# Optimization experiments

Measured on AMD Instinct MI355X. Metric: run time of the kernel, lower is better.

## Reference

```python
import jax, jax.numpy as jnp
import numpy as np

N_CVS = 4096
FEAT = 128
BATCH = 8192
K = 15
EPSILON = 0.9
E_MIN = 0.9 ** 10


def setup_inputs() -> dict:
    key = jax.random.key(0)
    k1, k2, k3 = jax.random.split(key, 3)
    x = jax.random.normal(k1, (BATCH, FEAT), dtype=jnp.float32)
    labels = jax.random.randint(k2, (BATCH,), 0, N_CVS, dtype=jnp.int64 if jax.config.jax_enable_x64 else jnp.int32)
    cvs = jax.random.normal(k3, (N_CVS, FEAT), dtype=jnp.float32)
    # module state buffers: identity-initialized edge / connectedness matrices
    edges = jnp.eye(N_CVS, dtype=jnp.float32)
    cv_connectedness = jnp.eye(N_CVS, dtype=jnp.float32)
    return {"x": x, "cvs": cvs, "edges": edges, "cv_connectedness": cv_connectedness, "labels": labels}


def reference(x, cvs, edges, cv_connectedness, labels):
    B = x.shape[0]
    N = cvs.shape[0]
    # squared pairwise distances (same ordering as cdist; x_cvs = cdist**2)
    d2 = (jnp.sum(x * x, axis=1)[:, None]
          + jnp.sum(cvs * cvs, axis=1)[None, :]
          - 2.0 * (x @ cvs.T))
    d2 = jnp.maximum(d2, 0.0)  # [B, N]

    # k nearest codevectors per sample (smallest distance first)
    _, knn = jax.lax.top_k(-d2, K)        # [B, K]
    closest = knn[:, 0]                    # [B]

    # visits per codevector (Counter over closest)
    visits = jnp.zeros((N,), dtype=jnp.float32).at[closest].add(1.0)
    # encounters[i, j] = visits[i]
    encounters = jnp.broadcast_to(visits[:, None], (N, N))

    # closest_cv_encounters[closest[i], knn[i, k]] += 1
    rows = jnp.repeat(closest, K)
    cols = knn.reshape(-1)
    cce = jnp.zeros((N, N), dtype=jnp.float32).at[rows, cols].add(1.0)

    existence = cce > 0
    enc = jnp.maximum(encounters - cce, 0.0)

    # edge update (state): refresh visited edges, exponentially decay others
    edges_new = jnp.maximum(edges, existence.astype(edges.dtype))
    edges_new = edges_new * (EPSILON ** enc)
    edges_new = jnp.where(edges_new < E_MIN, 0.0, edges_new)

    # margin loss
    d_pos = jnp.sum((x - cvs[labels]) ** 2, axis=1)                  # [B]
    neigh_mask = (edges_new > 0) & (cv_connectedness < 1)            # [N, N]
    d_neg = d2 * neigh_mask[labels].astype(d2.dtype)                 # [B, N]
    e_neg = jnp.exp(-0.001 * d_neg) * (d_neg > 0)
    w = e_neg / jnp.sum(e_neg, axis=1, keepdims=True)
    w = jnp.where(jnp.isnan(w), 0.0, w)
    w = jax.lax.stop_gradient(w)
    mu = d_pos - jnp.sum(w * d_neg, axis=1)
    loss = jnp.sum(jnp.maximum(mu, 0.0)) / B
    return loss
```

## Files before the change

kernel.cpp:

```cpp
#include <hip/hip_runtime.h>
#include <math.h>

#define N_CVS   4096
#define FEAT    128
#define BATCH   8192
#define KNN_K   15
#define E_MIN_F 0.34867844f

typedef __attribute__((ext_vector_type(8))) short bf16x8;
typedef __attribute__((ext_vector_type(4))) float f32x4;
typedef __attribute__((ext_vector_type(4))) unsigned int u32x4;

__global__ void cvtnorm_kernel(const float* __restrict__ x, const float* __restrict__ cvs,
                               unsigned short* __restrict__ xb, unsigned short* __restrict__ cb,
                               float* __restrict__ x2, float* __restrict__ c2) {
    size_t tid = (size_t)blockIdx.x * 256 + threadIdx.x;
    size_t f = tid * 8;
    const float* src; unsigned short* dst; float* ndst; size_t row;
    if (f < (size_t)BATCH * FEAT) { src = x + f; dst = xb + f; row = f >> 7; ndst = x2 + row; }
    else {
        size_t g = f - (size_t)BATCH * FEAT;
        src = cvs + g; dst = cb + g; row = g >> 7; ndst = c2 + row;
    }
    float4 v0 = ((const float4*)src)[0];
    float4 v1 = ((const float4*)src)[1];
    float vv[8] = {v0.x, v0.y, v0.z, v0.w, v1.x, v1.y, v1.z, v1.w};
    bf16x8 o;
    float s = 0.f;
    #pragma unroll
    for (int i = 0; i < 8; ++i) {
        unsigned u = __float_as_uint(vv[i]);
        o[i] = (short)((u + 0x7fffu + ((u >> 16) & 1u)) >> 16);
        s += vv[i] * vv[i];
    }
    *(bf16x8*)dst = o;
    #pragma unroll
    for (int off = 1; off < 16; off <<= 1) s += __shfl_xor(s, off, 64);
    if ((threadIdx.x & 15) == 0) *ndst = s;
}

#define LROW 272
#define TROW 132
__global__ __launch_bounds__(256) void mfma_d2_kernel(
        const unsigned short* __restrict__ xb, const unsigned short* __restrict__ cb,
        const float* __restrict__ x2g, const float* __restrict__ c2g,
        float* __restrict__ d2) {
    __shared__ __align__(16) char lds[2 * 128 * LROW];
    char* Al = lds;
    char* Bl = lds + 128 * LROW;
    const int bi = blockIdx.y * 128;
    const int bj = blockIdx.x * 128;
    const int t  = threadIdx.x;

    #pragma unroll
    for (int i = 0; i < 8; ++i) {
        int f = t + i * 256;
        int row = f >> 4, g = f & 15;
        ulonglong2 va = *(const ulonglong2*)((const char*)(xb + (size_t)(bi + row) * FEAT) + g * 16);
        *(ulonglong2*)(Al + row * LROW + g * 16) = va;
        ulonglong2 vb = *(const ulonglong2*)((const char*)(cb + (size_t)(bj + row) * FEAT) + g * 16);
        *(ulonglong2*)(Bl + row * LROW + g * 16) = vb;
    }
    __syncthreads();

    const int lane = t & 63;
    const int wave = t >> 6;
    const int wr = (wave >> 1) * 64;
    const int wc = (wave & 1) * 64;
    const int l15 = lane & 15, quad = lane >> 4;

    f32x4 acc[4][4];
    #pragma unroll
    for (int i = 0; i < 4; ++i)
        #pragma unroll
        for (int j = 0; j < 4; ++j)
            acc[i][j] = (f32x4){0.f, 0.f, 0.f, 0.f};

    #pragma unroll
    for (int ks = 0; ks < 4; ++ks) {
        bf16x8 a[4], b[4];
        #pragma unroll
        for (int s = 0; s < 4; ++s) {
            a[s] = *(const bf16x8*)(Al + (wr + s * 16 + l15) * LROW + ks * 64 + quad * 16);
            b[s] = *(const bf16x8*)(Bl + (wc + s * 16 + l15) * LROW + ks * 64 + quad * 16);
        }
        #pragma unroll
        for (int si = 0; si < 4; ++si)
            #pragma unroll
            for (int sj = 0; sj < 4; ++sj)
                acc[si][sj] = __builtin_amdgcn_mfma_f32_16x16x32_bf16(a[si], b[sj], acc[si][sj], 0, 0, 0);
    }

    float c2v[4];
    #pragma unroll
    for (int sj = 0; sj < 4; ++sj) c2v[sj] = c2g[bj + wc + sj * 16 + l15];
    __syncthreads();
    float* tile = (float*)lds;
    #pragma unroll
    for (int si = 0; si < 4; ++si) {
        #pragma unroll
        for (int r = 0; r < 4; ++r) {
            int mloc = wr + si * 16 + quad * 4 + r;
            float xv = x2g[bi + mloc];
            #pragma unroll
            for (int sj = 0; sj < 4; ++sj) {
                float v = fmaxf(xv + c2v[sj] - 2.0f * acc[si][sj][r], 0.0f);
                tile[mloc * TROW + wc + sj * 16 + l15] = v;
            }
        }
    }
    __syncthreads();
    #pragma unroll
    for (int i = 0; i < 16; ++i) {
        int s4  = t + i * 256;
        int row = s4 >> 5;
        int c4  = (s4 & 31) * 4;
        float4 v = *(const float4*)&tile[row * TROW + c4];
        *(float4*)(d2 + (size_t)(bi + row) * N_CVS + bj + c4) = v;
    }
}

__global__ __launch_bounds__(256, 3) void topk_kernel(const float* __restrict__ d2,
                                                      int* __restrict__ visits,
                                                      unsigned int* __restrict__ cce8) {
    __shared__ unsigned long long cand[4][64];
    const int wv   = threadIdx.x >> 6;
    const int wid  = blockIdx.x * 4 + wv;
    const int lane = threadIdx.x & 63;
    const float* row = d2 + (size_t)wid * N_CVS;

    float4 v[16];
    #pragma unroll
    for (int i = 0; i < 16; ++i)
        v[i] = *(const float4*)(row + lane * 4 + i * 256);

    float mn = fminf(fminf(v[0].x, v[0].y), fminf(v[0].z, v[0].w));
    #pragma unroll
    for (int i = 1; i < 16; ++i)
        mn = fminf(mn, fminf(fminf(v[i].x, v[i].y), fminf(v[i].z, v[i].w)));

    float s = mn;
    #pragma unroll
    for (int k = 2; k <= 64; k <<= 1) {
        #pragma unroll
        for (int j = k >> 1; j > 0; j >>= 1) {
            float o = __shfl_xor(s, j, 64);
            bool lower = ((lane & j) == 0);
            bool asc   = ((lane & k) == 0);
            float lo = fminf(s, o), hi = fmaxf(s, o);
            s = (lower == asc) ? lo : hi;
        }
    }
    float T = __shfl(s, 15, 64);

    unsigned long long* cbuf = cand[wv];
    int base = 0;
    #pragma unroll
    for (int i = 0; i < 16; ++i) {
        float vv[4] = {v[i].x, v[i].y, v[i].z, v[i].w};
        #pragma unroll
        for (int c = 0; c < 4; ++c) {
            bool p = (vv[c] <= T);
            unsigned long long mask = __ballot(p);
            if (p) {
                int pos = base + __popcll(mask & ((1ULL << lane) - 1ULL));
                if (pos < 64)
                    cbuf[pos] = ((unsigned long long)__float_as_uint(vv[c]) << 32)
                              | (unsigned)(lane * 4 + i * 256 + c);
            }
            base += __popcll(mask);
        }
    }
    __builtin_amdgcn_wave_barrier();

    int knnv[KNN_K];
    if (base <= 64) {
        unsigned long long key = (lane < base) ? cbuf[lane] : ~0ULL;
        #pragma unroll
        for (int r = 0; r < KNN_K; ++r) {
            unsigned long long m = key;
            #pragma unroll
            for (int off = 32; off > 0; off >>= 1) {
                unsigned long long o = __shfl_xor(m, off, 64);
                m = (o < m) ? o : m;
            }
            knnv[r] = (int)(unsigned)(m & 0xffffffffu);
            if (key == m) key = ~0ULL;
        }
    } else {
        unsigned long long heap[15];
        #pragma unroll
        for (int k = 0; k < 15; ++k) heap[k] = ~0ULL;
        for (int i = 0; i < 16; ++i) {
            int j0 = lane * 4 + i * 256;
            float4 f4 = *(const float4*)(row + j0);
            float vv[4] = {f4.x, f4.y, f4.z, f4.w};
            #pragma unroll
            for (int c = 0; c < 4; ++c) {
                unsigned long long key =
                    ((unsigned long long)__float_as_uint(vv[c]) << 32) | (unsigned)(j0 + c);
                if (key < heap[14]) {
                    heap[14] = key;
                    #pragma unroll
                    for (int k = 14; k > 0; --k) {
                        unsigned long long a = heap[k-1], b = heap[k];
                        bool sw = b < a;
                        heap[k-1] = sw ? b : a;
                        heap[k]   = sw ? a : b;
                    }
                }
            }
        }
        #pragma unroll
        for (int r = 0; r < KNN_K; ++r) {
            unsigned long long cd = heap[0];
            unsigned long long m = cd;
            #pragma unroll
            for (int off = 32; off > 0; off >>= 1) {
                unsigned long long o = __shfl_xor(m, off, 64);
                m = (o < m) ? o : m;
            }
            knnv[r] = (int)(unsigned)(m & 0xffffffffu);
            if (cd == m) {
                #pragma unroll
                for (int k = 0; k < 14; ++k) heap[k] = heap[k+1];
                heap[14] = ~0ULL;
            }
        }
    }

    if (lane == 0) {
        int closest = knnv[0];
        atomicAdd(&visits[closest], 1);
        size_t cbase = (size_t)closest * N_CVS;
        #pragma unroll
        for (int k = 0; k < KNN_K; ++k) {
            size_t idx = cbase + knnv[k];
            atomicAdd((int*)&cce8[idx >> 2], 1 << ((idx & 3) * 8));
        }
    }
}

__global__ __launch_bounds__(256) void bits_kernel(
        const unsigned int* __restrict__ cce8, const int* __restrict__ visits,
        const float* __restrict__ edges, const float* __restrict__ conn,
        unsigned short* __restrict__ bits16) {
    const int row = blockIdx.x;
    const int t   = threadIdx.x;
    const int vis = visits[row];
    size_t eb = (size_t)row * N_CVS + t * 16;
    f32x4 e[4];
    #pragma unroll
    for (int q = 0; q < 4; ++q) e[q] = ((const f32x4*)(edges + eb))[q];
    u32x4 cw = ((const u32x4*)(cce8 + (size_t)row * 1024))[t];

    unsigned pre = 0;
    #pragma unroll
    for (int q = 0; q < 4; ++q) {
        #pragma unroll
        for (int s = 0; s < 4; ++s) {
            int cc = (cw[q] >> (s * 8)) & 0xff;
            float ev = e[q][s];
            float ex = (cc > 0) ? fmaxf(ev, 1.0f) : ev;
            bool p;
            if (ex == 1.0f) {
                p = (vis - cc) <= 9;
            } else if (ex > 0.0f) {
                float enc = fmaxf((float)(vis - cc), 0.0f);
                p = ex * powf(0.9f, enc) >= E_MIN_F;
            } else {
                p = false;
            }
            pre |= (unsigned)p << (q * 4 + s);
        }
    }
    unsigned m = 0;
    #pragma unroll
    for (int q = 0; q < 4; ++q) {
        unsigned pn = (pre >> (q * 4)) & 0xfu;
        if (pn) {
            f32x4 cv = ((const f32x4*)(conn + eb))[q];
            #pragma unroll
            for (int s = 0; s < 4; ++s)
                if (((pn >> s) & 1u) && (cv[s] < 1.0f)) m |= 1u << (q * 4 + s);
        }
    }
    bits16[(size_t)row * 256 + t] = (unsigned short)m;
}

__global__ void loss_kernel(const float* __restrict__ d2,
                            const unsigned long long* __restrict__ bits,
                            const int* __restrict__ labels, float* __restrict__ partial) {
    int wid  = blockIdx.x * 4 + (threadIdx.x >> 6);
    int lane = threadIdx.x & 63;
    int l = labels[wid];
    const unsigned long long* rb = bits + (size_t)l * 64;
    const float* row = d2 + (size_t)wid * N_CVS;
    float se = 0.f, sed = 0.f;
    unsigned long long w = rb[lane];
    while (w) {
        int c = __builtin_ctzll(w);
        w &= w - 1;
        int j = lane * 64 + c;
        float d = row[j];
        if (d > 0.f) {
            float ee = __expf(-0.001f * d);
            se += ee; sed += ee * d;
        }
    }
    #pragma unroll
    for (int off = 32; off > 0; off >>= 1) {
        se  += __shfl_xor(se,  off, 64);
        sed += __shfl_xor(sed, off, 64);
    }
    if (lane == 0) {
        float dpos = row[l];
        float wsum = se > 0.f ? sed / se : 0.f;
        float mu = dpos - wsum;
        partial[wid] = (mu > 0.f) ? mu : 0.f;
    }
}

__global__ void reduce_kernel(const float* __restrict__ partial, float* __restrict__ out) {
    int t = threadIdx.x;
    float s = 0.f;
    #pragma unroll
    for (int i = 0; i < BATCH / 256; ++i) s += partial[t + i * 256];
    #pragma unroll
    for (int off = 32; off > 0; off >>= 1) s += __shfl_xor(s, off, 64);
    __shared__ float wsum[4];
    if ((t & 63) == 0) wsum[t >> 6] = s;
    __syncthreads();
    if (t == 0) out[0] = (wsum[0] + wsum[1] + wsum[2] + wsum[3]) * (1.0f / BATCH);
}

extern "C" void kernel_launch(void* const* d_in, const int* in_sizes, int n_in,
                              void* d_out, int out_size, void* d_ws, size_t ws_size,
                              hipStream_t stream) {
    const float* x      = (const float*)d_in[0];
    const float* cvs    = (const float*)d_in[1];
    const float* edges  = (const float*)d_in[2];
    const float* conn   = (const float*)d_in[3];
    const int*   labels = (const int*)d_in[4];

    char* p = (char*)d_ws;
    float* d2 = (float*)p;                  p += (size_t)BATCH * N_CVS * 4;
    int* visits = (int*)p;                  p += (size_t)N_CVS * 4;
    unsigned int* cce8 = (unsigned int*)p;  p += (size_t)N_CVS * N_CVS;
    unsigned long long* bits = (unsigned long long*)p;
                                            p += (size_t)N_CVS * 64 * 8;
    float* x2 = (float*)p;                  p += (size_t)BATCH * 4;
    float* c2 = (float*)p;                  p += (size_t)N_CVS * 4;
    unsigned short* xb = (unsigned short*)p; p += (size_t)BATCH * FEAT * 2;
    unsigned short* cb = (unsigned short*)p; p += (size_t)N_CVS * FEAT * 2;
    float* partial = (float*)p;             p += (size_t)BATCH * 4;

    hipMemsetAsync(visits, 0, (size_t)N_CVS * 4 + (size_t)N_CVS * N_CVS, stream);

    cvtnorm_kernel<<<(BATCH + N_CVS) * FEAT / 8 / 256, 256, 0, stream>>>(x, cvs, xb, cb, x2, c2);
    mfma_d2_kernel<<<dim3(N_CVS / 128, BATCH / 128), 256, 0, stream>>>(xb, cb, x2, c2, d2);
    topk_kernel   <<<BATCH / 4, 256, 0, stream>>>(d2, visits, cce8);
    bits_kernel   <<<N_CVS, 256, 0, stream>>>(
                      cce8, visits, edges, conn, (unsigned short*)bits);
    loss_kernel   <<<BATCH / 4, 256, 0, stream>>>(d2, bits, labels, partial);
    reduce_kernel <<<1, 256, 0, stream>>>(partial, (float*)d_out);
}
```

Baseline: 219.0 us.

## Fuse distance GEMM with streaming top-k and recompute loss distances on the fly

The bf16 MFMA distance computation is merged with k-nearest selection. Each 512-thread block keeps 32 x rows resident, streams codevector tiles through a double-buffered LDS, and keeps a running top-15 list per row using a shared candidate buffer with a threshold. This removes the 128 MB d2 matrix write and re-read. The loss kernel now recomputes the needed distances in fp32 directly from x and cvs for neighbour-mask bits only, so it no longer depends on d2. The cost is a per-tile __syncthreads loop with a serial insertion by 32 threads, low MFMA work per tile, and only 256 blocks.

```diff
diff --git a/kernel.cpp b/kernel.cpp
--- a/kernel.cpp
+++ b/kernel.cpp
@@ -10,6 +10,7 @@
 typedef __attribute__((ext_vector_type(8))) short bf16x8;
 typedef __attribute__((ext_vector_type(4))) float f32x4;
 typedef __attribute__((ext_vector_type(4))) unsigned int u32x4;
+typedef unsigned long long ull;
 
 __global__ void cvtnorm_kernel(const float* __restrict__ x, const float* __restrict__ cvs,
                                unsigned short* __restrict__ xb, unsigned short* __restrict__ cb,
@@ -39,203 +40,138 @@
     if ((threadIdx.x & 15) == 0) *ndst = s;
 }
 
-#define LROW 272
-#define TROW 132
-__global__ __launch_bounds__(256) void mfma_d2_kernel(
+#define LROW  272
+#define BROWS 32
+#define CAP   64
+#define NTILE (N_CVS / 128)
+
+__global__ __launch_bounds__(512, 2) void mfma_topk_kernel(
         const unsigned short* __restrict__ xb, const unsigned short* __restrict__ cb,
         const float* __restrict__ x2g, const float* __restrict__ c2g,
-        float* __restrict__ d2) {
-    __shared__ __align__(16) char lds[2 * 128 * LROW];
-    char* Al = lds;
-    char* Bl = lds + 128 * LROW;
-    const int bi = blockIdx.y * 128;
-    const int bj = blockIdx.x * 128;
+        int* __restrict__ visits, unsigned int* __restrict__ cce8) {
+    __shared__ __align__(16) char Bl[2][128 * LROW];
+    __shared__ __align__(16) char Al[BROWS * LROW];
+    __shared__ ull cand[BROWS][CAP];
+    __shared__ ull kT[BROWS];
+    __shared__ int cnt[BROWS];
+    __shared__ int ofl[BROWS];
+
     const int t  = threadIdx.x;
-
-    #pragma unroll
-    for (int i = 0; i < 8; ++i) {
-        int f = t + i * 256;
-        int row = f >> 4, g = f & 15;
-        ulonglong2 va = *(const ulonglong2*)((const char*)(xb + (size_t)(bi + row) * FEAT) + g * 16);
-        *(ulonglong2*)(Al + row * LROW + g * 16) = va;
-        ulonglong2 vb = *(const ulonglong2*)((const char*)(cb + (size_t)(bj + row) * FEAT) + g * 16);
-        *(ulonglong2*)(Bl + row * LROW + g * 16) = vb;
-    }
+    const int bi = blockIdx.x * BROWS;
+
+    {
+        int row = t >> 4, g = t & 15;
+        *(ulonglong2*)(Al + row * LROW + g * 16) =
+            *(const ulonglong2*)((const char*)(xb + (size_t)(bi + row) * FEAT) + g * 16);
+    }
+    #pragma unroll
+    for (int i = 0; i < 4; ++i) {
+        int f = t + i * 512, row = f >> 4, g = f & 15;
+        *(ulonglong2*)(Bl[0] + row * LROW + g * 16) =
+            *(const ulonglong2*)((const char*)(cb + (size_t)row * FEAT) + g * 16);
+    }
+    if (t < BROWS) { cnt[t] = 0; kT[t] = ~0ULL; ofl[t] = 0; }
     __syncthreads();
 
     const int lane = t & 63;
-    const int wave = t >> 6;
-    const int wr = (wave >> 1) * 64;
-    const int wc = (wave & 1) * 64;
-    const int l15 = lane & 15, quad = lane >> 4;
-
-    f32x4 acc[4][4];
-    #pragma unroll
-    for (int i = 0; i < 4; ++i)
-        #pragma unroll
-        for (int j = 0; j < 4; ++j)
-            acc[i][j] = (f32x4){0.f, 0.f, 0.f, 0.f};
-
-    #pragma unroll
-    for (int ks = 0; ks < 4; ++ks) {
-        bf16x8 a[4], b[4];
-        #pragma unroll
-        for (int s = 0; s < 4; ++s) {
-            a[s] = *(const bf16x8*)(Al + (wr + s * 16 + l15) * LROW + ks * 64 + quad * 16);
-            b[s] = *(const bf16x8*)(Bl + (wc + s * 16 + l15) * LROW + ks * 64 + quad * 16);
-        }
-        #pragma unroll
-        for (int si = 0; si < 4; ++si)
-            #pragma unroll
-            for (int sj = 0; sj < 4; ++sj)
-                acc[si][sj] = __builtin_amdgcn_mfma_f32_16x16x32_bf16(a[si], b[sj], acc[si][sj], 0, 0, 0);
-    }
-
-    float c2v[4];
-    #pragma unroll
-    for (int sj = 0; sj < 4; ++sj) c2v[sj] = c2g[bj + wc + sj * 16 + l15];
-    __syncthreads();
-    float* tile = (float*)lds;
-    #pragma unroll
-    for (int si = 0; si < 4; ++si) {
-        #pragma unroll
-        for (int r = 0; r < 4; ++r) {
-            int mloc = wr + si * 16 + quad * 4 + r;
-            float xv = x2g[bi + mloc];
-            #pragma unroll
-            for (int sj = 0; sj < 4; ++sj) {
-                float v = fmaxf(xv + c2v[sj] - 2.0f * acc[si][sj][r], 0.0f);
-                tile[mloc * TROW + wc + sj * 16 + l15] = v;
-            }
-        }
-    }
-    __syncthreads();
-    #pragma unroll
-    for (int i = 0; i < 16; ++i) {
-        int s4  = t + i * 256;
-        int row = s4 >> 5;
-        int c4  = (s4 & 31) * 4;
-        float4 v = *(const float4*)&tile[row * TROW + c4];
-        *(float4*)(d2 + (size_t)(bi + row) * N_CVS + bj + c4) = v;
-    }
-}
-
-__global__ __launch_bounds__(256, 3) void topk_kernel(const float* __restrict__ d2,
-                                                      int* __restrict__ visits,
-                                                      unsigned int* __restrict__ cce8) {
-    __shared__ unsigned long long cand[4][64];
-    const int wv   = threadIdx.x >> 6;
-    const int wid  = blockIdx.x * 4 + wv;
-    const int lane = threadIdx.x & 63;
-    const float* row = d2 + (size_t)wid * N_CVS;
-
-    float4 v[16];
-    #pragma unroll
-    for (int i = 0; i < 16; ++i)
-        v[i] = *(const float4*)(row + lane * 4 + i * 256);
-
-    float mn = fminf(fminf(v[0].x, v[0].y), fminf(v[0].z, v[0].w));
-    #pragma unroll
-    for (int i = 1; i < 16; ++i)
-        mn = fminf(mn, fminf(fminf(v[i].x, v[i].y), fminf(v[i].z, v[i].w)));
-
-    float s = mn;
-    #pragma unroll
-    for (int k = 2; k <= 64; k <<= 1) {
-        #pragma unroll
-        for (int j = k >> 1; j > 0; j >>= 1) {
-            float o = __shfl_xor(s, j, 64);
-            bool lower = ((lane & j) == 0);
-            bool asc   = ((lane & k) == 0);
-            float lo = fminf(s, o), hi = fmaxf(s, o);
-            s = (lower == asc) ? lo : hi;
-        }
-    }
-    float T = __shfl(s, 15, 64);
-
-    unsigned long long* cbuf = cand[wv];
-    int base = 0;
-    #pragma unroll
-    for (int i = 0; i < 16; ++i) {
-        float vv[4] = {v[i].x, v[i].y, v[i].z, v[i].w};
-        #pragma unroll
-        for (int c = 0; c < 4; ++c) {
-            bool p = (vv[c] <= T);
-            unsigned long long mask = __ballot(p);
-            if (p) {
-                int pos = base + __popcll(mask & ((1ULL << lane) - 1ULL));
-                if (pos < 64)
-                    cbuf[pos] = ((unsigned long long)__float_as_uint(vv[c]) << 32)
-                              | (unsigned)(lane * 4 + i * 256 + c);
-            }
-            base += __popcll(mask);
-        }
-    }
-    __builtin_amdgcn_wave_barrier();
-
-    int knnv[KNN_K];
-    if (base <= 64) {
-        unsigned long long key = (lane < base) ? cbuf[lane] : ~0ULL;
-        #pragma unroll
-        for (int r = 0; r < KNN_K; ++r) {
-            unsigned long long m = key;
-            #pragma unroll
-            for (int off = 32; off > 0; off >>= 1) {
-                unsigned long long o = __shfl_xor(m, off, 64);
-                m = (o < m) ? o : m;
-            }
-            knnv[r] = (int)(unsigned)(m & 0xffffffffu);
-            if (key == m) key = ~0ULL;
-        }
-    } else {
-        unsigned long long heap[15];
-        #pragma unroll
-        for (int k = 0; k < 15; ++k) heap[k] = ~0ULL;
-        for (int i = 0; i < 16; ++i) {
-            int j0 = lane * 4 + i * 256;
-            float4 f4 = *(const float4*)(row + j0);
-            float vv[4] = {f4.x, f4.y, f4.z, f4.w};
-            #pragma unroll
-            for (int c = 0; c < 4; ++c) {
-                unsigned long long key =
-                    ((unsigned long long)__float_as_uint(vv[c]) << 32) | (unsigned)(j0 + c);
-                if (key < heap[14]) {
-                    heap[14] = key;
-                    #pragma unroll
-                    for (int k = 14; k > 0; --k) {
-                        unsigned long long a = heap[k-1], b = heap[k];
-                        bool sw = b < a;
-                        heap[k-1] = sw ? b : a;
-                        heap[k]   = sw ? a : b;
+    const int w    = t >> 6;
+    const int l15  = lane & 15, quad = lane >> 4;
+
+    bf16x8 a[2][4];
+    float  x2r[2][4];
+    #pragma unroll
+    for (int si = 0; si < 2; ++si) {
+        #pragma unroll
+        for (int ks = 0; ks < 4; ++ks)
+            a[si][ks] = *(const bf16x8*)(Al + (si * 16 + l15) * LROW + ks * 64 + quad * 16);
+        #pragma unroll
+        for (int r = 0; r < 4; ++r)
+            x2r[si][r] = x2g[bi + si * 16 + quad * 4 + r];
+    }
+
+    ull lst[15];
+    #pragma unroll
+    for (int i = 0; i < 15; ++i) lst[i] = ~0ULL;
+
+    for (int tj = 0; tj < NTILE; ++tj) {
+        const char* cur = Bl[tj & 1];
+        if (tj + 1 < NTILE) {
+            char* nxt = Bl[(tj + 1) & 1];
+            const int cjn = (tj + 1) * 128;
+            #pragma unroll
+            for (int i = 0; i < 4; ++i) {
+                int f = t + i * 512, row = f >> 4, g = f & 15;
+                *(ulonglong2*)(nxt + row * LROW + g * 16) =
+                    *(const ulonglong2*)((const char*)(cb + (size_t)(cjn + row) * FEAT) + g * 16);
+            }
+        }
+
+        f32x4 acc[2] = {(f32x4){0.f,0.f,0.f,0.f}, (f32x4){0.f,0.f,0.f,0.f}};
+        #pragma unroll
+        for (int ks = 0; ks < 4; ++ks) {
+            bf16x8 b = *(const bf16x8*)(cur + (w * 16 + l15) * LROW + ks * 64 + quad * 16);
+            acc[0] = __builtin_amdgcn_mfma_f32_16x16x32_bf16(a[0][ks], b, acc[0], 0, 0, 0);
+            acc[1] = __builtin_amdgcn_mfma_f32_16x16x32_bf16(a[1][ks], b, acc[1], 0, 0, 0);
+        }
+
+        const int col = tj * 128 + w * 16 + l15;
+        const float c2v = c2g[col];
+        ull key[2][4];
+        #pragma unroll
+        for (int si = 0; si < 2; ++si)
+            #pragma unroll
+            for (int r = 0; r < 4; ++r) {
+                float v = fmaxf(x2r[si][r] + c2v - 2.0f * acc[si][r], 0.0f);
+                key[si][r] = ((ull)__float_as_uint(v) << 32) | (unsigned)col;
+            }
+
+        unsigned am = 0;
+        int round = 0, more;
+        do {
+            #pragma unroll
+            for (int si = 0; si < 2; ++si)
+                #pragma unroll
+                for (int r = 0; r < 4; ++r) {
+                    int rl = si * 16 + quad * 4 + r;
+                    unsigned bit = 1u << (si * 4 + r);
+                    if (!(am & bit) && (round == 0 || ofl[rl]) && key[si][r] < kT[rl]) {
+                        int pos = atomicAdd(&cnt[rl], 1);
+                        if (pos < CAP) { cand[rl][pos] = key[si][r]; am |= bit; }
                     }
                 }
-            }
-        }
-        #pragma unroll
-        for (int r = 0; r < KNN_K; ++r) {
-            unsigned long long cd = heap[0];
-            unsigned long long m = cd;
-            #pragma unroll
-            for (int off = 32; off > 0; off >>= 1) {
-                unsigned long long o = __shfl_xor(m, off, 64);
-                m = (o < m) ? o : m;
-            }
-            knnv[r] = (int)(unsigned)(m & 0xffffffffu);
-            if (cd == m) {
-                #pragma unroll
-                for (int k = 0; k < 14; ++k) heap[k] = heap[k+1];
-                heap[14] = ~0ULL;
-            }
-        }
-    }
-
-    if (lane == 0) {
-        int closest = knnv[0];
+            __syncthreads();
+            int of = 0;
+            if (t < BROWS) {
+                int n = cnt[t];
+                if (n) {
+                    int m = n < CAP ? n : CAP;
+                    for (int i = 0; i < m; ++i) {
+                        ull k = cand[t][i];
+                        #pragma unroll
+                        for (int q = 0; q < 15; ++q) {
+                            ull lo = k < lst[q] ? k : lst[q];
+                            ull hi = k < lst[q] ? lst[q] : k;
+                            lst[q] = lo; k = hi;
+                        }
+                    }
+                    kT[t]  = lst[14];
+                    cnt[t] = 0;
+                    of = (n > CAP);
+                }
+                ofl[t] = of;
+            }
+            more = __syncthreads_or(of);
+            ++round;
+        } while (more);
+    }
+
+    if (t < BROWS) {
+        int closest = (int)(unsigned)(lst[0] & 0xffffffffu);
         atomicAdd(&visits[closest], 1);
         size_t cbase = (size_t)closest * N_CVS;
         #pragma unroll
         for (int k = 0; k < KNN_K; ++k) {
-            size_t idx = cbase + knnv[k];
+            size_t idx = cbase + (unsigned)(lst[k] & 0xffffffffu);
             atomicAdd((int*)&cce8[idx >> 2], 1 << ((idx & 3) * 8));
         }
     }
@@ -288,33 +224,48 @@
     bits16[(size_t)row * 256 + t] = (unsigned short)m;
 }
 
-__global__ void loss_kernel(const float* __restrict__ d2,
-                            const unsigned long long* __restrict__ bits,
-                            const int* __restrict__ labels, float* __restrict__ partial) {
+__global__ __launch_bounds__(256) void loss_kernel(
+        const float* __restrict__ x, const float* __restrict__ cvs,
+        const ull* __restrict__ bits, const int* __restrict__ labels,
+        float* __restrict__ partial) {
     int wid  = blockIdx.x * 4 + (threadIdx.x >> 6);
     int lane = threadIdx.x & 63;
     int l = labels[wid];
-    const unsigned long long* rb = bits + (size_t)l * 64;
-    const float* row = d2 + (size_t)wid * N_CVS;
+    float2 xv = ((const float2*)(x + (size_t)wid * FEAT))[lane];
+    ull myw = bits[(size_t)l * 64 + lane];
+
+    float dpos;
+    {
+        float2 c = ((const float2*)(cvs + (size_t)l * FEAT))[lane];
+        float d0 = xv.x - c.x, d1 = xv.y - c.y;
+        float s = d0 * d0 + d1 * d1;
+        #pragma unroll
+        for (int off = 32; off > 0; off >>= 1) s += __shfl_xor(s, off, 64);
+        dpos = s;
+    }
+
     float se = 0.f, sed = 0.f;
-    unsigned long long w = rb[lane];
-    while (w) {
-        int c = __builtin_ctzll(w);
-        w &= w - 1;
-        int j = lane * 64 + c;
-        float d = row[j];
-        if (d > 0.f) {
-            float ee = __expf(-0.001f * d);
-            se += ee; sed += ee * d;
-        }
-    }
-    #pragma unroll
-    for (int off = 32; off > 0; off >>= 1) {
-        se  += __shfl_xor(se,  off, 64);
-        sed += __shfl_xor(sed, off, 64);
+    ull nz = __ballot(myw != 0ULL);
+    while (nz) {
+        int wd = __builtin_ctzll(nz);
+        nz &= nz - 1;
+        ull word = __shfl(myw, wd, 64);
+        while (word) {
+            int b = __builtin_ctzll(word);
+            word &= word - 1;
+            int j = wd * 64 + b;
+            float2 c = ((const float2*)(cvs + (size_t)j * FEAT))[lane];
+            float d0 = xv.x - c.x, d1 = xv.y - c.y;
+            float s = d0 * d0 + d1 * d1;
+            #pragma unroll
+            for (int off = 32; off > 0; off >>= 1) s += __shfl_xor(s, off, 64);
+            if (s > 0.f) {
+                float ee = __expf(-0.001f * s);
+                se += ee; sed += ee * s;
+            }
+        }
     }
     if (lane == 0) {
-        float dpos = row[l];
         float wsum = se > 0.f ? sed / se : 0.f;
         float mu = dpos - wsum;
         partial[wid] = (mu > 0.f) ? mu : 0.f;
@@ -344,11 +295,9 @@
     const int*   labels = (const int*)d_in[4];
 
     char* p = (char*)d_ws;
-    float* d2 = (float*)p;                  p += (size_t)BATCH * N_CVS * 4;
     int* visits = (int*)p;                  p += (size_t)N_CVS * 4;
     unsigned int* cce8 = (unsigned int*)p;  p += (size_t)N_CVS * N_CVS;
-    unsigned long long* bits = (unsigned long long*)p;
-                                            p += (size_t)N_CVS * 64 * 8;
+    ull* bits = (ull*)p;                    p += (size_t)N_CVS * 64 * 8;
     float* x2 = (float*)p;                  p += (size_t)BATCH * 4;
     float* c2 = (float*)p;                  p += (size_t)N_CVS * 4;
     unsigned short* xb = (unsigned short*)p; p += (size_t)BATCH * FEAT * 2;
@@ -357,11 +306,9 @@
 
     hipMemsetAsync(visits, 0, (size_t)N_CVS * 4 + (size_t)N_CVS * N_CVS, stream);
 
-    cvtnorm_kernel<<<(BATCH + N_CVS) * FEAT / 8 / 256, 256, 0, stream>>>(x, cvs, xb, cb, x2, c2);
-    mfma_d2_kernel<<<dim3(N_CVS / 128, BATCH / 128), 256, 0, stream>>>(xb, cb, x2, c2, d2);
-    topk_kernel   <<<BATCH / 4, 256, 0, stream>>>(d2, visits, cce8);
-    bits_kernel   <<<N_CVS, 256, 0, stream>>>(
-                      cce8, visits, edges, conn, (unsigned short*)bits);
-    loss_kernel   <<<BATCH / 4, 256, 0, stream>>>(d2, bits, labels, partial);
-    reduce_kernel <<<1, 256, 0, stream>>>(partial, (float*)d_out);
-}
+    cvtnorm_kernel  <<<(BATCH + N_CVS) * FEAT / 8 / 256, 256, 0, stream>>>(x, cvs, xb, cb, x2, c2);
+    mfma_topk_kernel<<<BATCH / BROWS, 512, 0, stream>>>(xb, cb, x2, c2, visits, cce8);
+    bits_kernel     <<<N_CVS, 256, 0, stream>>>(cce8, visits, edges, conn, (unsigned short*)bits);
+    loss_kernel     <<<BATCH / 4, 256, 0, stream>>>(x, cvs, bits, labels, partial);
+    reduce_kernel   <<<1, 256, 0, stream>>>(partial, (float*)d_out);
+}
```

Result: slower. 344.6 us (+57.3%).
